# Performance work log

Hardware: AMD Instinct MI355X
Metric: run time of the kernel (lower is better)

The kernel has to match this reference:

```python
import jax, jax.numpy as jnp
import numpy as np

N_NODES = 50000
N_EDGES = 600000
HIDDEN = 128


def _sage_conv(x, src, dst, W_l, W_r, b):
    """PyG SAGEConv with mean aggregation:
    out_i = W_l @ mean_{j in N(i)} x_j + W_r @ x_i + b
    src/dst: [E] edge endpoints (message flows src -> dst).
    """
    msg = x[src]  # [E, d] gather
    agg = jax.ops.segment_sum(msg, dst, num_segments=N_NODES)  # [N, d]
    cnt = jax.ops.segment_sum(jnp.ones((src.shape[0],), x.dtype), dst,
                              num_segments=N_NODES)  # [N]
    mean = agg / jnp.maximum(cnt, 1.0)[:, None]
    return mean @ W_l.T + x @ W_r.T + b


def setup_inputs() -> dict:
    key = jax.random.key(0)
    ks = jax.random.split(key, 12)
    x = jax.random.normal(ks[0], (N_NODES, HIDDEN), dtype=jnp.float32)
    edge_index = jax.random.randint(ks[1], (2, N_EDGES), 0, N_NODES, dtype=jnp.int64)
    scale = 1.0 / np.sqrt(HIDDEN)
    inp = {"x": x, "edge_index": edge_index}
    for i, layer in enumerate(["1", "2", "3"]):
        inp["Wl" + layer] = jax.random.uniform(ks[2 + 3 * i], (HIDDEN, HIDDEN),
                                               minval=-scale, maxval=scale, dtype=jnp.float32)
        inp["Wr" + layer] = jax.random.uniform(ks[3 + 3 * i], (HIDDEN, HIDDEN),
                                               minval=-scale, maxval=scale, dtype=jnp.float32)
        inp["b" + layer] = jax.random.uniform(ks[4 + 3 * i], (HIDDEN,),
                                              minval=-scale, maxval=scale, dtype=jnp.float32)
    return inp


def reference(x, edge_index, Wl1, Wr1, b1, Wl2, Wr2, b2, Wl3, Wr3, b3):
    src, dst = edge_index[0], edge_index[1]
    h = jax.nn.relu(_sage_conv(x, src, dst, Wl1, Wr1, b1))
    h = _sage_conv(h, src, dst, Wl2, Wr2, b2)
    h = _sage_conv(h, src, dst, Wl3, Wr3, b3)
    return h
```

## Files before the change

kernel.cpp:

```cpp
#include <hip/hip_runtime.h>
#include <hip/hip_bf16.h>

#define N_NODES 50000
#define N_EDGES 600000
#define HID 128

typedef __attribute__((ext_vector_type(8))) short s8v;
typedef __attribute__((ext_vector_type(8))) unsigned short u8v;
typedef __attribute__((ext_vector_type(4))) float f4v;

__device__ __forceinline__ unsigned short f2bf(float x) {
    unsigned u = __float_as_uint(x);
    unsigned r = u + 0x7FFFu + ((u >> 16) & 1u);
    return (unsigned short)(r >> 16);
}
__device__ __forceinline__ float bf2f(unsigned short u) {
    return __uint_as_float((unsigned)u << 16);
}
__device__ __forceinline__ void split_bf(float x, unsigned short& hi, unsigned short& lo) {
    hi = f2bf(x);
    lo = f2bf(x - bf2f(hi));
}

__device__ __forceinline__ int detect_m64_block(const void* edges) {
    __shared__ int m64s;
    if (threadIdx.x == 0) m64s = 1;
    __syncthreads();
    const int* p = (const int*)edges;
    if (p[2 * threadIdx.x + 1] != 0) m64s = 0;
    __syncthreads();
    return m64s;
}

__device__ __forceinline__ int edge_at(const void* edges, int mode64, long long idx) {
    return mode64 ? (int)((const long long*)edges)[idx] : ((const int*)edges)[idx];
}

__global__ void count_deg(const void* __restrict__ edges, int* __restrict__ deg) {
    int m = detect_m64_block(edges);
    int e = blockIdx.x * 256 + threadIdx.x;
    if (e >= N_EDGES) return;
    int d = edge_at(edges, m, (long long)N_EDGES + e);
    if ((unsigned)d < (unsigned)N_NODES) atomicAdd(&deg[d], 1);
}

__global__ void scan_block(const int* __restrict__ deg, int* __restrict__ offs,
                           int* __restrict__ blocksum) {
    __shared__ int sm[256];
    int i = blockIdx.x * 256 + threadIdx.x;
    int v = (i < N_NODES) ? deg[i] : 0;
    sm[threadIdx.x] = v;
    __syncthreads();
    #pragma unroll
    for (int s = 1; s < 256; s <<= 1) {
        int t = (threadIdx.x >= (unsigned)s) ? sm[threadIdx.x - s] : 0;
        __syncthreads();
        sm[threadIdx.x] += t;
        __syncthreads();
    }
    if (i < N_NODES) offs[i] = sm[threadIdx.x] - v;
    if (threadIdx.x == 255) blocksum[blockIdx.x] = sm[255];
}

__global__ void scan_add(int* __restrict__ offs, int* __restrict__ cursor,
                         const int* __restrict__ blocksum, int nblocks) {
    __shared__ int sm[256];
    int v = ((int)threadIdx.x < nblocks) ? blocksum[threadIdx.x] : 0;
    sm[threadIdx.x] = v;
    __syncthreads();
    #pragma unroll
    for (int s = 1; s < 256; s <<= 1) {
        int t = (threadIdx.x >= (unsigned)s) ? sm[threadIdx.x - s] : 0;
        __syncthreads();
        sm[threadIdx.x] += t;
        __syncthreads();
    }
    const int pre = (blockIdx.x == 0) ? 0 : sm[blockIdx.x - 1];
    const int total = sm[nblocks - 1];
    int i = blockIdx.x * 256 + threadIdx.x;
    if (i < N_NODES) {
        int o = offs[i] + pre;
        offs[i] = o;
        cursor[i] = o;
    }
    if (i == 0) offs[N_NODES] = total;
}

__global__ void fill_csr(const void* __restrict__ edges, int* __restrict__ cursor,
                         int* __restrict__ csr) {
    int m = detect_m64_block(edges);
    int e = blockIdx.x * 256 + threadIdx.x;
    if (e >= N_EDGES) return;
    int d = edge_at(edges, m, (long long)N_EDGES + e);
    int s = edge_at(edges, m, (long long)e);
    if ((unsigned)d >= (unsigned)N_NODES || (unsigned)s >= (unsigned)N_NODES) return;
    int pos = atomicAdd(&cursor[d], 1);
    csr[pos] = s;
}

__global__ void prep(const float* __restrict__ m0, const float* __restrict__ m1,
                     const float* __restrict__ m2, const float* __restrict__ m3,
                     const float* __restrict__ m4, const float* __restrict__ m5,
                     unsigned short* __restrict__ whi, unsigned short* __restrict__ wlo,
                     const float* __restrict__ x, unsigned short* __restrict__ xhi,
                     unsigned short* __restrict__ xlo, int n4) {
    int i = blockIdx.x * 256 + threadIdx.x;
    if (i < 6 * HID * HID) {
        int mat = i >> 14, off = i & 16383;
        const float* src = mat == 0 ? m0 : mat == 1 ? m1 : mat == 2 ? m2
                         : mat == 3 ? m3 : mat == 4 ? m4 : m5;
        unsigned short h, l;
        split_bf(src[off], h, l);
        whi[i] = h; wlo[i] = l;
    }
    if (i < n4) {
        float4 v = ((const float4*)x)[i];
        ushort4 h, l;
        split_bf(v.x, h.x, l.x);
        split_bf(v.y, h.y, l.y);
        split_bf(v.z, h.z, l.z);
        split_bf(v.w, h.w, l.w);
        ((ushort4*)xhi)[i] = h;
        ((ushort4*)xlo)[i] = l;
    }
}

__global__ __launch_bounds__(256) void aggregate_bf16(const unsigned short* __restrict__ h,
                                                      const int* __restrict__ offs,
                                                      const int* __restrict__ csr,
                                                      unsigned short* __restrict__ mhi) {
    const int sub  = threadIdx.x & 15;
    const int node = blockIdx.x * 16 + (threadIdx.x >> 4);
    if (node >= N_NODES) return;
    const int beg = offs[node], end = offs[node + 1];
    float a[8] = {0.f, 0.f, 0.f, 0.f, 0.f, 0.f, 0.f, 0.f};
    int p = beg;
    for (; p + 8 <= end; p += 8) {
        int s0 = csr[p],     s1 = csr[p + 1], s2 = csr[p + 2], s3 = csr[p + 3];
        int s4 = csr[p + 4], s5 = csr[p + 5], s6 = csr[p + 6], s7 = csr[p + 7];
        u8v v0 = *(const u8v*)(h + (size_t)s0 * HID + sub * 8);
        u8v v1 = *(const u8v*)(h + (size_t)s1 * HID + sub * 8);
        u8v v2 = *(const u8v*)(h + (size_t)s2 * HID + sub * 8);
        u8v v3 = *(const u8v*)(h + (size_t)s3 * HID + sub * 8);
        u8v v4 = *(const u8v*)(h + (size_t)s4 * HID + sub * 8);
        u8v v5 = *(const u8v*)(h + (size_t)s5 * HID + sub * 8);
        u8v v6 = *(const u8v*)(h + (size_t)s6 * HID + sub * 8);
        u8v v7 = *(const u8v*)(h + (size_t)s7 * HID + sub * 8);
        #pragma unroll
        for (int j = 0; j < 8; ++j)
            a[j] += ((bf2f(v0[j]) + bf2f(v1[j])) + (bf2f(v2[j]) + bf2f(v3[j])))
                  + ((bf2f(v4[j]) + bf2f(v5[j])) + (bf2f(v6[j]) + bf2f(v7[j])));
    }
    if (p + 4 <= end) {
        int s0 = csr[p], s1 = csr[p + 1], s2 = csr[p + 2], s3 = csr[p + 3];
        u8v v0 = *(const u8v*)(h + (size_t)s0 * HID + sub * 8);
        u8v v1 = *(const u8v*)(h + (size_t)s1 * HID + sub * 8);
        u8v v2 = *(const u8v*)(h + (size_t)s2 * HID + sub * 8);
        u8v v3 = *(const u8v*)(h + (size_t)s3 * HID + sub * 8);
        #pragma unroll
        for (int j = 0; j < 8; ++j)
            a[j] += (bf2f(v0[j]) + bf2f(v1[j])) + (bf2f(v2[j]) + bf2f(v3[j]));
        p += 4;
    }
    for (; p < end; ++p) {
        int s = csr[p];
        u8v v = *(const u8v*)(h + (size_t)s * HID + sub * 8);
        #pragma unroll
        for (int j = 0; j < 8; ++j) a[j] += bf2f(v[j]);
    }
    const float inv = 1.0f / fmaxf((float)(end - beg), 1.0f);
    u8v hh;
    #pragma unroll
    for (int j = 0; j < 8; ++j) hh[j] = f2bf(a[j] * inv);
    *(u8v*)(mhi + (size_t)node * HID + sub * 8) = hh;
}

template <int RELU, int FINAL>
__global__ __launch_bounds__(256) void sage_mfma(
    const unsigned short* __restrict__ Mhi,
    const unsigned short* __restrict__ Hhi, const unsigned short* __restrict__ Hlo,
    const unsigned short* __restrict__ Whi, const unsigned short* __restrict__ Wlo,
    const float* __restrict__ bias,
    unsigned short* __restrict__ ohi, unsigned short* __restrict__ olo,
    float* __restrict__ of32) {
    __shared__ short BhS[128 * 72];
    __shared__ short BlS[128 * 72];
    const int tid = threadIdx.x;
    const int wave = tid >> 6, lane = tid & 63;
    const int mIdx = lane & 15, q = lane >> 4;
    const int wrow = (wave & 1) * 64, wcol = (wave >> 1) * 64;
    const int rowBase = blockIdx.x * 128;

    size_t aoff[4];
    #pragma unroll
    for (int t = 0; t < 4; ++t) {
        int node = rowBase + wrow + t * 16 + mIdx;
        if (node > N_NODES - 1) node = N_NODES - 1;
        aoff[t] = (size_t)node * HID + q * 8;
    }
    const int bcol = tid & 127;
    const int bseg = (tid >> 7) * 32;

    f4v acc[4][4];
    #pragma unroll
    for (int a = 0; a < 4; ++a)
        #pragma unroll
        for (int b = 0; b < 4; ++b) acc[a][b] = (f4v){0.f, 0.f, 0.f, 0.f};

    s8v Ah[2][4], Al[2][4];
    auto loadA = [&](int i, int buf) {
        const int kc = (i & 3) * 32;
        if (i < 4) {
            #pragma unroll
            for (int t = 0; t < 4; ++t)
                Ah[buf][t] = *(const s8v*)(Mhi + aoff[t] + kc);
        } else {
            #pragma unroll
            for (int t = 0; t < 4; ++t) {
                Ah[buf][t] = *(const s8v*)(Hhi + aoff[t] + kc);
                Al[buf][t] = *(const s8v*)(Hlo + aoff[t] + kc);
            }
        }
    };

    loadA(0, 0);
    #pragma unroll 1
    for (int panel = 0; panel < 4; ++panel) {
        const int ph = panel >> 1;
        const int kb = (panel & 1) * 64;
        const unsigned short* Wh_ = Whi + ph * HID * HID;
        const unsigned short* Wl_ = Wlo + ph * HID * HID;
        __syncthreads();
        {
            const unsigned short* sh = Wh_ + bcol * HID + kb + bseg;
            const unsigned short* sl = Wl_ + bcol * HID + kb + bseg;
            short* dh = BhS + bcol * 72 + bseg;
            short* dl = BlS + bcol * 72 + bseg;
            #pragma unroll
            for (int j = 0; j < 4; ++j) {
                *(s8v*)(dh + j * 8) = *(const s8v*)(sh + j * 8);
                *(s8v*)(dl + j * 8) = *(const s8v*)(sl + j * 8);
            }
        }
        __syncthreads();
        #pragma unroll
        for (int c = 0; c < 2; ++c) {
            const int i = panel * 2 + c;
            if (i < 7) loadA(i + 1, (i + 1) & 1);
            const int kc2 = c * 32;
            s8v Bh_f[4], Bl_f[4];
            #pragma unroll
            for (int nt = 0; nt < 4; ++nt) {
                const int a = (wcol + nt * 16 + mIdx) * 72 + kc2 + q * 8;
                Bh_f[nt] = *(const s8v*)(BhS + a);
                Bl_f[nt] = *(const s8v*)(BlS + a);
            }
            const int buf = i & 1;
            if (panel < 2) {
                #pragma unroll
                for (int mt = 0; mt < 4; ++mt)
                    #pragma unroll
                    for (int nt = 0; nt < 4; ++nt) {
                        acc[mt][nt] = __builtin_amdgcn_mfma_f32_16x16x32_bf16(
                            Ah[buf][mt], Bh_f[nt], acc[mt][nt], 0, 0, 0);
                        acc[mt][nt] = __builtin_amdgcn_mfma_f32_16x16x32_bf16(
                            Ah[buf][mt], Bl_f[nt], acc[mt][nt], 0, 0, 0);
                    }
            } else {
                #pragma unroll
                for (int mt = 0; mt < 4; ++mt)
                    #pragma unroll
                    for (int nt = 0; nt < 4; ++nt) {
                        acc[mt][nt] = __builtin_amdgcn_mfma_f32_16x16x32_bf16(
                            Ah[buf][mt], Bh_f[nt], acc[mt][nt], 0, 0, 0);
                        acc[mt][nt] = __builtin_amdgcn_mfma_f32_16x16x32_bf16(
                            Al[buf][mt], Bh_f[nt], acc[mt][nt], 0, 0, 0);
                        acc[mt][nt] = __builtin_amdgcn_mfma_f32_16x16x32_bf16(
                            Ah[buf][mt], Bl_f[nt], acc[mt][nt], 0, 0, 0);
                    }
            }
        }
    }

    float bv[4];
    #pragma unroll
    for (int nt = 0; nt < 4; ++nt) bv[nt] = bias[wcol + nt * 16 + mIdx];

    #pragma unroll
    for (int mt = 0; mt < 4; ++mt)
        #pragma unroll
        for (int r = 0; r < 4; ++r) {
            int node = rowBase + wrow + mt * 16 + q * 4 + r;
            if (node < N_NODES) {
                #pragma unroll
                for (int nt = 0; nt < 4; ++nt) {
                    int feat = wcol + nt * 16 + mIdx;
                    float v = acc[mt][nt][r] + bv[nt];
                    if (RELU) v = fmaxf(v, 0.f);
                    size_t oidx = (size_t)node * HID + feat;
                    if (FINAL) {
                        of32[oidx] = v;
                    } else {
                        unsigned short hh, ll;
                        split_bf(v, hh, ll);
                        ohi[oidx] = hh;
                        olo[oidx] = ll;
                    }
                }
            }
        }
}

extern "C" void kernel_launch(void* const* d_in, const int* in_sizes, int n_in,
                              void* d_out, int out_size, void* d_ws, size_t ws_size,
                              hipStream_t stream) {
    const float* x   = (const float*)d_in[0];
    const void* edges = d_in[1];
    const float* Wl1 = (const float*)d_in[2];
    const float* Wr1 = (const float*)d_in[3];
    const float* b1  = (const float*)d_in[4];
    const float* Wl2 = (const float*)d_in[5];
    const float* Wr2 = (const float*)d_in[6];
    const float* b2  = (const float*)d_in[7];
    const float* Wl3 = (const float*)d_in[8];
    const float* Wr3 = (const float*)d_in[9];
    const float* b3  = (const float*)d_in[10];
    float* out = (float*)d_out;

    char* ws = (char*)d_ws;
    size_t off = 0;
    auto alloc = [&](size_t bytes) -> void* {
        void* p = (void*)(ws + off);
        off += (bytes + 255) & ~(size_t)255;
        return p;
    };
    typedef unsigned short u16;
    const size_t FEAT = (size_t)N_NODES * HID;
    int* deg      = (int*)alloc((size_t)N_NODES * 4);
    int* offs     = (int*)alloc((size_t)(N_NODES + 1) * 4);
    int* cursor   = (int*)alloc((size_t)N_NODES * 4);
    int* blocksum = (int*)alloc(256 * 4);
    int* csr      = (int*)alloc((size_t)N_EDGES * 4);
    u16* whi      = (u16*)alloc((size_t)6 * HID * HID * 2);
    u16* wlo      = (u16*)alloc((size_t)6 * HID * HID * 2);
    u16* xhi      = (u16*)alloc(FEAT * 2);
    u16* xlo      = (u16*)alloc(FEAT * 2);
    u16* h1hi     = (u16*)alloc(FEAT * 2);
    u16* h1lo     = (u16*)alloc(FEAT * 2);
    u16* mhi      = (u16*)alloc(FEAT * 2);
    (void)ws_size; (void)in_sizes; (void)n_in; (void)out_size;

    const int EB = (N_EDGES + 255) / 256;
    const int NB = (N_NODES + 255) / 256;
    const int AGG_B = (N_NODES + 15) / 16;
    const int GEMM_B = (N_NODES + 127) / 128;
    const int PREP_B = ((int)(FEAT / 4) + 255) / 256;

    hipMemsetAsync(deg, 0, (size_t)N_NODES * 4, stream);
    count_deg<<<EB, 256, 0, stream>>>(edges, deg);
    scan_block<<<NB, 256, 0, stream>>>(deg, offs, blocksum);
    scan_add<<<NB, 256, 0, stream>>>(offs, cursor, blocksum, NB);
    fill_csr<<<EB, 256, 0, stream>>>(edges, cursor, csr);
    prep<<<PREP_B, 256, 0, stream>>>(Wl1, Wr1, Wl2, Wr2, Wl3, Wr3, whi, wlo,
                                     x, xhi, xlo, (int)(FEAT / 4));

    aggregate_bf16<<<AGG_B, 256, 0, stream>>>(xhi, offs, csr, mhi);
    sage_mfma<1, 0><<<GEMM_B, 256, 0, stream>>>(mhi, xhi, xlo,
        whi, wlo, b1, h1hi, h1lo, (float*)nullptr);
    aggregate_bf16<<<AGG_B, 256, 0, stream>>>(h1hi, offs, csr, mhi);
    sage_mfma<0, 0><<<GEMM_B, 256, 0, stream>>>(mhi, h1hi, h1lo,
        whi + 2 * HID * HID, wlo + 2 * HID * HID, b2, xhi, xlo, (float*)nullptr);
    aggregate_bf16<<<AGG_B, 256, 0, stream>>>(xhi, offs, csr, mhi);
    sage_mfma<0, 1><<<GEMM_B, 256, 0, stream>>>(mhi, xhi, xlo,
        whi + 4 * HID * HID, wlo + 4 * HID * HID, b3,
        (u16*)nullptr, (u16*)nullptr, out);
}
```

Before: 356.1 us.

## Drop lo-part of activations, halve GEMM row tile, deepen A prefetch

Activations are now stored only as a bf16 hi part. The lo buffers for x and the hidden layers are removed, along with the Al×Bh MFMA term in the self term. The GEMM row tile is halved to 64 rows per block, which doubles the block count, and A fragments are prefetched three steps ahead through a 4-deep register ring. This cuts memory traffic and MFMA work, but the output is less precise because the x@W_r term loses the activation's low-order correction.

```diff
diff --git a/kernel.cpp b/kernel.cpp
--- a/kernel.cpp
+++ b/kernel.cpp
@@ -103,7 +103,7 @@
                      const float* __restrict__ m4, const float* __restrict__ m5,
                      unsigned short* __restrict__ whi, unsigned short* __restrict__ wlo,
                      const float* __restrict__ x, unsigned short* __restrict__ xhi,
-                     unsigned short* __restrict__ xlo, int n4) {
+                     int n4) {
     int i = blockIdx.x * 256 + threadIdx.x;
     if (i < 6 * HID * HID) {
         int mat = i >> 14, off = i & 16383;
@@ -115,13 +115,9 @@
     }
     if (i < n4) {
         float4 v = ((const float4*)x)[i];
-        ushort4 h, l;
-        split_bf(v.x, h.x, l.x);
-        split_bf(v.y, h.y, l.y);
-        split_bf(v.z, h.z, l.z);
-        split_bf(v.w, h.w, l.w);
+        ushort4 h;
+        h.x = f2bf(v.x); h.y = f2bf(v.y); h.z = f2bf(v.z); h.w = f2bf(v.w);
         ((ushort4*)xhi)[i] = h;
-        ((ushort4*)xlo)[i] = l;
     }
 }
 
@@ -177,23 +173,21 @@
 
 template <int RELU, int FINAL>
 __global__ __launch_bounds__(256) void sage_mfma(
-    const unsigned short* __restrict__ Mhi,
-    const unsigned short* __restrict__ Hhi, const unsigned short* __restrict__ Hlo,
+    const unsigned short* __restrict__ Mhi, const unsigned short* __restrict__ Hhi,
     const unsigned short* __restrict__ Whi, const unsigned short* __restrict__ Wlo,
     const float* __restrict__ bias,
-    unsigned short* __restrict__ ohi, unsigned short* __restrict__ olo,
-    float* __restrict__ of32) {
+    unsigned short* __restrict__ ohi, float* __restrict__ of32) {
     __shared__ short BhS[128 * 72];
     __shared__ short BlS[128 * 72];
     const int tid = threadIdx.x;
     const int wave = tid >> 6, lane = tid & 63;
     const int mIdx = lane & 15, q = lane >> 4;
-    const int wrow = (wave & 1) * 64, wcol = (wave >> 1) * 64;
-    const int rowBase = blockIdx.x * 128;
-
-    size_t aoff[4];
-    #pragma unroll
-    for (int t = 0; t < 4; ++t) {
+    const int wrow = (wave & 1) * 32, wcol = (wave >> 1) * 64;
+    const int rowBase = blockIdx.x * 64;
+
+    size_t aoff[2];
+    #pragma unroll
+    for (int t = 0; t < 2; ++t) {
         int node = rowBase + wrow + t * 16 + mIdx;
         if (node > N_NODES - 1) node = N_NODES - 1;
         aoff[t] = (size_t)node * HID + q * 8;
@@ -201,29 +195,23 @@
     const int bcol = tid & 127;
     const int bseg = (tid >> 7) * 32;
 
-    f4v acc[4][4];
-    #pragma unroll
-    for (int a = 0; a < 4; ++a)
+    f4v acc[2][4];
+    #pragma unroll
+    for (int a = 0; a < 2; ++a)
         #pragma unroll
         for (int b = 0; b < 4; ++b) acc[a][b] = (f4v){0.f, 0.f, 0.f, 0.f};
 
-    s8v Ah[2][4], Al[2][4];
-    auto loadA = [&](int i, int buf) {
+    s8v A4[4][2];
+    auto loadA = [&](int i) {
+        const unsigned short* src = (i < 4) ? Mhi : Hhi;
         const int kc = (i & 3) * 32;
-        if (i < 4) {
-            #pragma unroll
-            for (int t = 0; t < 4; ++t)
-                Ah[buf][t] = *(const s8v*)(Mhi + aoff[t] + kc);
-        } else {
-            #pragma unroll
-            for (int t = 0; t < 4; ++t) {
-                Ah[buf][t] = *(const s8v*)(Hhi + aoff[t] + kc);
-                Al[buf][t] = *(const s8v*)(Hlo + aoff[t] + kc);
-            }
-        }
+        const int buf = i & 3;
+        #pragma unroll
+        for (int t = 0; t < 2; ++t)
+            A4[buf][t] = *(const s8v*)(src + aoff[t] + kc);
     };
 
-    loadA(0, 0);
+    loadA(0); loadA(1); loadA(2);
     #pragma unroll 1
     for (int panel = 0; panel < 4; ++panel) {
         const int ph = panel >> 1;
@@ -246,7 +234,7 @@
         #pragma unroll
         for (int c = 0; c < 2; ++c) {
             const int i = panel * 2 + c;
-            if (i < 7) loadA(i + 1, (i + 1) & 1);
+            if (i + 3 < 8) loadA(i + 3);
             const int kc2 = c * 32;
             s8v Bh_f[4], Bl_f[4];
             #pragma unroll
@@ -255,30 +243,16 @@
                 Bh_f[nt] = *(const s8v*)(BhS + a);
                 Bl_f[nt] = *(const s8v*)(BlS + a);
             }
-            const int buf = i & 1;
-            if (panel < 2) {
+            const int buf = i & 3;
+            #pragma unroll
+            for (int mt = 0; mt < 2; ++mt)
                 #pragma unroll
-                for (int mt = 0; mt < 4; ++mt)
-                    #pragma unroll
-                    for (int nt = 0; nt < 4; ++nt) {
-                        acc[mt][nt] = __builtin_amdgcn_mfma_f32_16x16x32_bf16(
-                            Ah[buf][mt], Bh_f[nt], acc[mt][nt], 0, 0, 0);
-                        acc[mt][nt] = __builtin_amdgcn_mfma_f32_16x16x32_bf16(
-                            Ah[buf][mt], Bl_f[nt], acc[mt][nt], 0, 0, 0);
-                    }
-            } else {
-                #pragma unroll
-                for (int mt = 0; mt < 4; ++mt)
-                    #pragma unroll
-                    for (int nt = 0; nt < 4; ++nt) {
-                        acc[mt][nt] = __builtin_amdgcn_mfma_f32_16x16x32_bf16(
-                            Ah[buf][mt], Bh_f[nt], acc[mt][nt], 0, 0, 0);
-                        acc[mt][nt] = __builtin_amdgcn_mfma_f32_16x16x32_bf16(
-                            Al[buf][mt], Bh_f[nt], acc[mt][nt], 0, 0, 0);
-                        acc[mt][nt] = __builtin_amdgcn_mfma_f32_16x16x32_bf16(
-                            Ah[buf][mt], Bl_f[nt], acc[mt][nt], 0, 0, 0);
-                    }
-            }
+                for (int nt = 0; nt < 4; ++nt) {
+                    acc[mt][nt] = __builtin_amdgcn_mfma_f32_16x16x32_bf16(
+                        A4[buf][mt], Bh_f[nt], acc[mt][nt], 0, 0, 0);
+                    acc[mt][nt] = __builtin_amdgcn_mfma_f32_16x16x32_bf16(
+                        A4[buf][mt], Bl_f[nt], acc[mt][nt], 0, 0, 0);
+                }
         }
     }
 
@@ -287,7 +261,7 @@
     for (int nt = 0; nt < 4; ++nt) bv[nt] = bias[wcol + nt * 16 + mIdx];
 
     #pragma unroll
-    for (int mt = 0; mt < 4; ++mt)
+    for (int mt = 0; mt < 2; ++mt)
         #pragma unroll
         for (int r = 0; r < 4; ++r) {
             int node = rowBase + wrow + mt * 16 + q * 4 + r;
@@ -298,14 +272,8 @@
                     float v = acc[mt][nt][r] + bv[nt];
                     if (RELU) v = fmaxf(v, 0.f);
                     size_t oidx = (size_t)node * HID + feat;
-                    if (FINAL) {
-                        of32[oidx] = v;
-                    } else {
-                        unsigned short hh, ll;
-                        split_bf(v, hh, ll);
-                        ohi[oidx] = hh;
-                        olo[oidx] = ll;
-                    }
+                    if (FINAL) of32[oidx] = v;
+                    else       ohi[oidx] = f2bf(v);
                 }
             }
         }
@@ -344,16 +312,14 @@
     u16* whi      = (u16*)alloc((size_t)6 * HID * HID * 2);
     u16* wlo      = (u16*)alloc((size_t)6 * HID * HID * 2);
     u16* xhi      = (u16*)alloc(FEAT * 2);
-    u16* xlo      = (u16*)alloc(FEAT * 2);
     u16* h1hi     = (u16*)alloc(FEAT * 2);
-    u16* h1lo     = (u16*)alloc(FEAT * 2);
     u16* mhi      = (u16*)alloc(FEAT * 2);
     (void)ws_size; (void)in_sizes; (void)n_in; (void)out_size;
 
     const int EB = (N_EDGES + 255) / 256;
     const int NB = (N_NODES + 255) / 256;
     const int AGG_B = (N_NODES + 15) / 16;
-    const int GEMM_B = (N_NODES + 127) / 128;
+    const int GEMM_B = (N_NODES + 63) / 64;
     const int PREP_B = ((int)(FEAT / 4) + 255) / 256;
 
     hipMemsetAsync(deg, 0, (size_t)N_NODES * 4, stream);
@@ -362,16 +328,16 @@
     scan_add<<<NB, 256, 0, stream>>>(offs, cursor, blocksum, NB);
     fill_csr<<<EB, 256, 0, stream>>>(edges, cursor, csr);
     prep<<<PREP_B, 256, 0, stream>>>(Wl1, Wr1, Wl2, Wr2, Wl3, Wr3, whi, wlo,
-                                     x, xhi, xlo, (int)(FEAT / 4));
+                                     x, xhi, (int)(FEAT / 4));
 
     aggregate_bf16<<<AGG_B, 256, 0, stream>>>(xhi, offs, csr, mhi);
-    sage_mfma<1, 0><<<GEMM_B, 256, 0, stream>>>(mhi, xhi, xlo,
-        whi, wlo, b1, h1hi, h1lo, (float*)nullptr);
+    sage_mfma<1, 0><<<GEMM_B, 256, 0, stream>>>(mhi, xhi,
+        whi, wlo, b1, h1hi, (float*)nullptr);
     aggregate_bf16<<<AGG_B, 256, 0, stream>>>(h1hi, offs, csr, mhi);
-    sage_mfma<0, 0><<<GEMM_B, 256, 0, stream>>>(mhi, h1hi, h1lo,
-        whi + 2 * HID * HID, wlo + 2 * HID * HID, b2, xhi, xlo, (float*)nullptr);
+    sage_mfma<0, 0><<<GEMM_B, 256, 0, stream>>>(mhi, h1hi,
+        whi + 2 * HID * HID, wlo + 2 * HID * HID, b2, xhi, (float*)nullptr);
     aggregate_bf16<<<AGG_B, 256, 0, stream>>>(xhi, offs, csr, mhi);
-    sage_mfma<0, 1><<<GEMM_B, 256, 0, stream>>>(mhi, xhi, xlo,
+    sage_mfma<0, 1><<<GEMM_B, 256, 0, stream>>>(mhi, xhi,
         whi + 4 * HID * HID, wlo + 4 * HID * HID, b3,
-        (u16*)nullptr, (u16*)nullptr, out);
-}
+        (u16*)nullptr, out);
+}
```

After: 1.203 ms. 238% more time.
